# Kernel tuning notes

Measured on AMD Instinct MI355X. Metric: run time of the kernel, lower is better.

Reference implementation:

```python
import jax, jax.numpy as jnp
import numpy as np

B, S, D, N = 8, 4096, 768, 64


def setup_inputs() -> dict:
    key = jax.random.key(0)
    k1, k2 = jax.random.split(key)
    word_vectors = jax.random.normal(k1, (B, S, D), dtype=jnp.float32)
    sent_rep_token_ids = jnp.sort(jax.random.randint(k2, (B, N), 0, S), axis=1)
    sent_rep_mask = jnp.ones((B, N), dtype=jnp.float32)
    # sent_lengths: each row must sum exactly to S (torch.split contract).
    rng = np.random.default_rng(0)
    lens = np.stack([
        np.diff(np.concatenate([[0], np.sort(rng.choice(np.arange(1, S), N - 1, replace=False)), [S]]))
        for _ in range(B)
    ])
    sent_lengths = jnp.asarray(lens, dtype=jnp.int64) if jax.config.jax_enable_x64 else jnp.asarray(lens, dtype=jnp.int32)
    sent_lengths_mask = jnp.ones((B, N), dtype=jnp.float32)
    return {
        "word_vectors": word_vectors,
        "sent_rep_token_ids": sent_rep_token_ids,
        "sent_rep_mask": sent_rep_mask,
        "sent_lengths": sent_lengths,
        "sent_lengths_mask": sent_lengths_mask,
    }


def reference(word_vectors, sent_rep_token_ids, sent_rep_mask, sent_lengths, sent_lengths_mask):
    b, s, d = word_vectors.shape
    n = sent_lengths.shape[1]
    dt = word_vectors.dtype

    # --- sent_rep_tokens branch: gather CLS-style token per sentence ---
    rep_vec = jnp.take_along_axis(word_vectors, sent_rep_token_ids[:, :, None], axis=1)  # [B,N,D]
    rep_vec = rep_vec * sent_rep_mask[:, :, None].astype(dt)

    # --- mean_tokens branch: ragged per-segment mean via segment_sum ---
    ends = jnp.cumsum(sent_lengths, axis=1)                      # [B,N] exclusive-end offsets
    pos = jnp.arange(s)
    seg = jax.vmap(lambda e: jnp.searchsorted(e, pos, side='right'))(ends)  # [B,S] segment id per token
    gseg = (seg + jnp.arange(b)[:, None] * n).reshape(-1)        # global segment ids [B*S]
    flat = word_vectors.reshape(b * s, d)
    sums = jax.ops.segment_sum(flat, gseg, num_segments=b * n).reshape(b, n, d)
    counts = jax.ops.segment_sum((flat != 0).astype(dt), gseg, num_segments=b * n).reshape(b, n, d)
    mean = sums / jnp.maximum(counts, 1)
    # fallback to word_vectors[0,0] when a segment has zero nonzero entries (original semantics)
    all_zero = (counts.sum(axis=-1) == 0)                        # [B,N]
    mean = jnp.where(all_zero[:, :, None], word_vectors[0, 0], mean)
    mean_vec = mean * sent_lengths_mask[:, :, None].astype(dt)

    out_vectors = jnp.concatenate([rep_vec, mean_vec], axis=1)   # [B,2N,D]
    out_masks = jnp.concatenate([sent_rep_mask, sent_lengths_mask], axis=1)  # [B,2N]
    return out_vectors, out_masks
```

## Files before the change

### kernel.cpp

```cpp
#include <hip/hip_runtime.h>

#define BB 8
#define SS 4096
#define DD 768
#define NN 64
#define D4 (DD / 4)
#define CHT 128
#define MAXCH 96
#define NREC (BB * MAXCH)

typedef float nfloat4 __attribute__((ext_vector_type(4)));

__global__ __launch_bounds__(256) void chunk_kernel(
    const float* __restrict__ wv,
    const int* __restrict__ lens,
    float* __restrict__ ws_sum,
    unsigned char* __restrict__ ws_cnt)
{
    const int cidx = blockIdx.x;
    const int b    = blockIdx.y;
    const int g    = blockIdx.z;
    const int tid  = threadIdx.x;
    const int lane = tid & 63;
    const int w    = tid >> 6;

    const int l    = lens[b * NN + lane];
    const int nchl = (l + CHT - 1) >> 7;
    int inclen = l, inch = nchl;
    #pragma unroll
    for (int off = 1; off < 64; off <<= 1) {
        int a = __shfl_up(inclen, off); if (lane >= off) inclen += a;
        int c = __shfl_up(inch,   off); if (lane >= off) inch   += c;
    }
    const int total_ch = __shfl(inch, 63);
    if (cidx >= total_ch) return;

    unsigned long long m = __ballot(inch > cidx);
    const int n         = __ffsll(m) - 1;
    const int seg_len   = __shfl(l, n);
    const int seg_start = __shfl(inclen, n) - seg_len;
    const int ch_base   = __shfl(inch, n) - __shfl(nchl, n);
    const int t0 = seg_start + (cidx - ch_base) * CHT;
    const int t1 = min(seg_start + seg_len, t0 + CHT);

    const int col4 = g * 64 + lane;
    const nfloat4* base = (const nfloat4*)wv + (size_t)b * SS * D4 + col4;

    float4 s = make_float4(0.f, 0.f, 0.f, 0.f);
    float4 c = make_float4(0.f, 0.f, 0.f, 0.f);
    #pragma unroll 8
    for (int t = t0 + w; t < t1; t += 4) {
        nfloat4 v = __builtin_nontemporal_load(base + (size_t)t * D4);
        s.x += v.x; s.y += v.y; s.z += v.z; s.w += v.w;
        c.x += (v.x != 0.f) ? 1.f : 0.f;
        c.y += (v.y != 0.f) ? 1.f : 0.f;
        c.z += (v.z != 0.f) ? 1.f : 0.f;
        c.w += (v.w != 0.f) ? 1.f : 0.f;
    }

    __shared__ float4 s_s[4][64];
    __shared__ float4 s_c[4][64];
    s_s[w][lane] = s;
    s_c[w][lane] = c;
    __syncthreads();

    if (tid < 64) {
        float4 S = make_float4(0.f, 0.f, 0.f, 0.f);
        float4 C = make_float4(0.f, 0.f, 0.f, 0.f);
        #pragma unroll
        for (int j = 0; j < 4; ++j) {
            float4 a = s_s[j][tid], d = s_c[j][tid];
            S.x += a.x; S.y += a.y; S.z += a.z; S.w += a.w;
            C.x += d.x; C.y += d.y; C.z += d.z; C.w += d.w;
        }
        const size_t rec = (size_t)(b * MAXCH + cidx);
        ((float4*)ws_sum)[rec * D4 + g * 64 + tid] = S;
        uchar4 u;
        u.x = (unsigned char)C.x; u.y = (unsigned char)C.y;
        u.z = (unsigned char)C.z; u.w = (unsigned char)C.w;
        ((uchar4*)ws_cnt)[rec * D4 + g * 64 + tid] = u;
    }
}

__global__ __launch_bounds__(256) void finalize_kernel(
    const float* __restrict__ wv,
    const int* __restrict__ rep_ids,
    const float* __restrict__ rep_mask,
    const int* __restrict__ lens,
    const float* __restrict__ len_mask,
    const float* __restrict__ ws_sum,
    const unsigned char* __restrict__ ws_cnt,
    float* __restrict__ out)
{
    __shared__ float s_part[4];
    __shared__ int s_info[2];
    const int sgid = blockIdx.x;
    const int b = sgid >> 6, n = sgid & 63;
    const int tid = threadIdx.x;
    const int lane = tid & 63;

    if (tid < 64) {
        const int l    = lens[b * NN + tid];
        const int nchl = (l + CHT - 1) >> 7;
        int inch = nchl;
        #pragma unroll
        for (int off = 1; off < 64; off <<= 1) {
            int a = __shfl_up(inch, off); if (lane >= off) inch += a;
        }
        if (tid == n) { s_info[0] = inch - nchl; s_info[1] = nchl; }
    }
    __syncthreads();
    const int ch_base = s_info[0];
    const int K       = s_info[1];
    const bool active = tid < D4;

    float4 S = make_float4(0,0,0,0), C = S;
    if (active) {
        for (int k = 0; k < K; ++k) {
            const size_t rec = (size_t)(b * MAXCH + ch_base + k);
            float4 sv = ((const float4*)ws_sum)[rec * D4 + tid];
            uchar4 cv = ((const uchar4*)ws_cnt)[rec * D4 + tid];
            S.x += sv.x; S.y += sv.y; S.z += sv.z; S.w += sv.w;
            C.x += (float)cv.x; C.y += (float)cv.y;
            C.z += (float)cv.z; C.w += (float)cv.w;
        }
    }

    float tot = C.x + C.y + C.z + C.w;
    #pragma unroll
    for (int off = 32; off; off >>= 1) tot += __shfl_xor(tot, off);
    if ((tid & 63) == 0) s_part[tid >> 6] = tot;
    __syncthreads();
    const float total = s_part[0] + s_part[1] + s_part[2] + s_part[3];

    if (active) {
        float4 mean;
        mean.x = S.x / fmaxf(C.x, 1.f);
        mean.y = S.y / fmaxf(C.y, 1.f);
        mean.z = S.z / fmaxf(C.z, 1.f);
        mean.w = S.w / fmaxf(C.w, 1.f);
        if (total == 0.f) mean = ((const float4*)wv)[tid];

        const float lm = len_mask[sgid];
        mean.x *= lm; mean.y *= lm; mean.z *= lm; mean.w *= lm;

        float4* out4 = (float4*)out;
        out4[(size_t)(b * 2 * NN + NN + n) * D4 + tid] = mean;

        const int   rid = rep_ids[sgid];
        const float rm  = rep_mask[sgid];
        float4 rv = ((const float4*)wv)[(size_t)(b * SS + rid) * D4 + tid];
        rv.x *= rm; rv.y *= rm; rv.z *= rm; rv.w *= rm;
        out4[(size_t)(b * 2 * NN + n) * D4 + tid] = rv;

        if (tid == 0) {
            float* masks = out + (size_t)BB * 2 * NN * DD;
            masks[b * 2 * NN + n]      = rm;
            masks[b * 2 * NN + NN + n] = lm;
        }
    }
}

extern "C" void kernel_launch(void* const* d_in, const int* in_sizes, int n_in,
                              void* d_out, int out_size, void* d_ws, size_t ws_size,
                              hipStream_t stream) {
    const float* wv       = (const float*)d_in[0];
    const int*   rep_ids  = (const int*)d_in[1];
    const float* rep_mask = (const float*)d_in[2];
    const int*   lens     = (const int*)d_in[3];
    const float* len_mask = (const float*)d_in[4];
    float*       out      = (float*)d_out;
    float*         ws_sum = (float*)d_ws;
    unsigned char* ws_cnt = (unsigned char*)d_ws + (size_t)NREC * DD * 4;

    dim3 gridB(MAXCH, BB, 3);
    chunk_kernel<<<gridB, 256, 0, stream>>>(wv, lens, ws_sum, ws_cnt);
    finalize_kernel<<<BB * NN, 256, 0, stream>>>(wv, rep_ids, rep_mask, lens,
                                                 len_mask, ws_sum, ws_cnt, out);
}
```

Baseline: 157.3 us.

## Process full row width per block with 8 waves instead of splitting columns across grid

```diff
diff --git a/kernel.cpp b/kernel.cpp
--- a/kernel.cpp
+++ b/kernel.cpp
@@ -8,10 +8,12 @@
 #define CHT 128
 #define MAXCH 96
 #define NREC (BB * MAXCH)
+#define WAVES 8
+#define BLOCK (WAVES * 64)
 
 typedef float nfloat4 __attribute__((ext_vector_type(4)));
 
-__global__ __launch_bounds__(256) void chunk_kernel(
+__global__ __launch_bounds__(BLOCK) void chunk_kernel(
     const float* __restrict__ wv,
     const int* __restrict__ lens,
     float* __restrict__ ws_sum,
@@ -19,7 +21,6 @@
 {
     const int cidx = blockIdx.x;
     const int b    = blockIdx.y;
-    const int g    = blockIdx.z;
     const int tid  = threadIdx.x;
     const int lane = tid & 63;
     const int w    = tid >> 6;
@@ -43,42 +44,52 @@
     const int t0 = seg_start + (cidx - ch_base) * CHT;
     const int t1 = min(seg_start + seg_len, t0 + CHT);
 
-    const int col4 = g * 64 + lane;
-    const nfloat4* base = (const nfloat4*)wv + (size_t)b * SS * D4 + col4;
+    const nfloat4* base = (const nfloat4*)wv + (size_t)b * SS * D4;
 
-    float4 s = make_float4(0.f, 0.f, 0.f, 0.f);
-    float4 c = make_float4(0.f, 0.f, 0.f, 0.f);
-    #pragma unroll 8
-    for (int t = t0 + w; t < t1; t += 4) {
-        nfloat4 v = __builtin_nontemporal_load(base + (size_t)t * D4);
-        s.x += v.x; s.y += v.y; s.z += v.z; s.w += v.w;
-        c.x += (v.x != 0.f) ? 1.f : 0.f;
-        c.y += (v.y != 0.f) ? 1.f : 0.f;
-        c.z += (v.z != 0.f) ? 1.f : 0.f;
-        c.w += (v.w != 0.f) ? 1.f : 0.f;
+    float4 s0 = make_float4(0,0,0,0), s1 = s0, s2 = s0;
+    float4 c0 = s0, c1 = s0, c2 = s0;
+    #pragma unroll 2
+    for (int t = t0 + w; t < t1; t += WAVES) {
+        const nfloat4* row = base + (size_t)t * D4 + lane;
+        nfloat4 v0 = __builtin_nontemporal_load(row);
+        nfloat4 v1 = __builtin_nontemporal_load(row + 64);
+        nfloat4 v2 = __builtin_nontemporal_load(row + 128);
+        s0.x += v0.x; s0.y += v0.y; s0.z += v0.z; s0.w += v0.w;
+        s1.x += v1.x; s1.y += v1.y; s1.z += v1.z; s1.w += v1.w;
+        s2.x += v2.x; s2.y += v2.y; s2.z += v2.z; s2.w += v2.w;
+        c0.x += (v0.x != 0.f) ? 1.f : 0.f; c0.y += (v0.y != 0.f) ? 1.f : 0.f;
+        c0.z += (v0.z != 0.f) ? 1.f : 0.f; c0.w += (v0.w != 0.f) ? 1.f : 0.f;
+        c1.x += (v1.x != 0.f) ? 1.f : 0.f; c1.y += (v1.y != 0.f) ? 1.f : 0.f;
+        c1.z += (v1.z != 0.f) ? 1.f : 0.f; c1.w += (v1.w != 0.f) ? 1.f : 0.f;
+        c2.x += (v2.x != 0.f) ? 1.f : 0.f; c2.y += (v2.y != 0.f) ? 1.f : 0.f;
+        c2.z += (v2.z != 0.f) ? 1.f : 0.f; c2.w += (v2.w != 0.f) ? 1.f : 0.f;
     }
 
-    __shared__ float4 s_s[4][64];
-    __shared__ float4 s_c[4][64];
-    s_s[w][lane] = s;
-    s_c[w][lane] = c;
+    __shared__ float4 s_s[WAVES][D4];
+    __shared__ float4 s_c[WAVES][D4];
+    s_s[w][lane]       = s0;
+    s_s[w][64 + lane]  = s1;
+    s_s[w][128 + lane] = s2;
+    s_c[w][lane]       = c0;
+    s_c[w][64 + lane]  = c1;
+    s_c[w][128 + lane] = c2;
     __syncthreads();
 
-    if (tid < 64) {
-        float4 S = make_float4(0.f, 0.f, 0.f, 0.f);
-        float4 C = make_float4(0.f, 0.f, 0.f, 0.f);
+    if (tid < D4) {
+        float4 S = make_float4(0,0,0,0);
+        float4 C = make_float4(0,0,0,0);
         #pragma unroll
-        for (int j = 0; j < 4; ++j) {
+        for (int j = 0; j < WAVES; ++j) {
             float4 a = s_s[j][tid], d = s_c[j][tid];
             S.x += a.x; S.y += a.y; S.z += a.z; S.w += a.w;
             C.x += d.x; C.y += d.y; C.z += d.z; C.w += d.w;
         }
         const size_t rec = (size_t)(b * MAXCH + cidx);
-        ((float4*)ws_sum)[rec * D4 + g * 64 + tid] = S;
+        ((float4*)ws_sum)[rec * D4 + tid] = S;
         uchar4 u;
         u.x = (unsigned char)C.x; u.y = (unsigned char)C.y;
         u.z = (unsigned char)C.z; u.w = (unsigned char)C.w;
-        ((uchar4*)ws_cnt)[rec * D4 + g * 64 + tid] = u;
+        ((uchar4*)ws_cnt)[rec * D4 + tid] = u;
     }
 }
 
@@ -173,8 +184,8 @@
     float*         ws_sum = (float*)d_ws;
     unsigned char* ws_cnt = (unsigned char*)d_ws + (size_t)NREC * DD * 4;
 
-    dim3 gridB(MAXCH, BB, 3);
-    chunk_kernel<<<gridB, 256, 0, stream>>>(wv, lens, ws_sum, ws_cnt);
+    dim3 gridB(MAXCH, BB);
+    chunk_kernel<<<gridB, BLOCK, 0, stream>>>(wv, lens, ws_sum, ws_cnt);
     finalize_kernel<<<BB * NN, 256, 0, stream>>>(wv, rep_ids, rep_mask, lens,
                                                  len_mask, ws_sum, ws_cnt, out);
 }
```

After: 158.4 us. About the same (+0.7%).
